# Kernel tuning notes

Hardware: AMD Instinct MI355X
Metric: run time of the kernel (lower is better)

Reference implementation:

```python
import jax, jax.numpy as jnp
import numpy as np

B, S, D, H, DQK, DH = 2, 2048, 1024, 16, 64, 64

def setup_inputs() -> dict:
    key = jax.random.key(0)
    ks = jax.random.split(key, 9)
    return {
        "x":  jax.random.normal(ks[0], (B, S, D), jnp.float32),
        "Wq": jax.random.normal(ks[1], (H, D, DQK), jnp.float32) * (D ** -0.5),
        "bq": jax.random.normal(ks[2], (H, DQK), jnp.float32) * 0.02,
        "Wk": jax.random.normal(ks[3], (H, D, DQK), jnp.float32) * (D ** -0.5),
        "bk": jax.random.normal(ks[4], (H, DQK), jnp.float32) * 0.02,
        "Wv": jax.random.normal(ks[5], (H, D, DH), jnp.float32) * (D ** -0.5),
        "bv": jax.random.normal(ks[6], (H, DH), jnp.float32) * 0.02,
        "Wo": jax.random.normal(ks[7], (D, D), jnp.float32) * (D ** -0.5),
        "bo": jax.random.normal(ks[8], (D,), jnp.float32) * 0.02,
    }

def reference(x, Wq, bq, Wk, bk, Wv, bv, Wo, bo):
    b, s, d = x.shape
    # per-head projections, all heads batched: [B,H,S,*]
    Q = jnp.einsum('bsd,hde->bhse', x, Wq) + bq[None, :, None, :]
    K = jnp.einsum('bsd,hde->bhse', x, Wk) + bk[None, :, None, :]
    V = jnp.einsum('bsd,hde->bhse', x, Wv) + bv[None, :, None, :]
    scores = jnp.einsum('bhse,bhte->bhst', Q, K) * (Q.shape[-1] ** -0.5)
    causal = jnp.tril(jnp.ones((s, s), bool))
    scores = jnp.where(causal, scores, -jnp.inf)  # mask add as in torch code
    attn = jax.nn.softmax(scores, axis=-1)        # dropout p=0 (eval)
    out = jnp.einsum('bhst,bhtd->bhsd', attn, V)
    # concat heads along feature dim (head order matches torch.cat)
    out = out.transpose(0, 2, 1, 3).reshape(b, s, -1)
    return out @ Wo + bo
```

## Files before the change

### kernel.cpp

```cpp
#include <hip/hip_runtime.h>
#include <stdint.h>

typedef __attribute__((ext_vector_type(8))) short bh8;
typedef __attribute__((ext_vector_type(4))) float f32x4;
typedef __attribute__((ext_vector_type(4))) unsigned short u16x4;
typedef __attribute__((ext_vector_type(8))) unsigned short u16x8;
typedef __attribute__((ext_vector_type(2))) unsigned int u32x2;

#define DEVI static __device__ __forceinline__

constexpr int B_ = 2, S_ = 2048, D_ = 1024, H_ = 16, E_ = 64;

constexpr size_t OFF_XB  = 0;
constexpr size_t OFF_WQT = OFF_XB  + (size_t)B_*S_*D_;
constexpr size_t OFF_WKT = OFF_WQT + (size_t)H_*E_*D_;
constexpr size_t OFF_WVT = OFF_WKT + (size_t)H_*E_*D_;
constexpr size_t OFF_WOT = OFF_WVT + (size_t)H_*E_*D_;
constexpr size_t OFF_Q   = OFF_WOT + (size_t)D_*D_;
constexpr size_t OFF_K   = OFF_Q   + (size_t)B_*H_*S_*E_;
constexpr size_t OFF_VT  = OFF_K   + (size_t)B_*H_*S_*E_;
constexpr size_t OFF_O   = OFF_VT  + (size_t)B_*H_*S_*E_;

DEVI unsigned short f2bf(float f) {
    union { float f; unsigned u; } v; v.f = f;
    unsigned u = v.u;
    return (unsigned short)((u + 0x7fffu + ((u >> 16) & 1u)) >> 16);
}

DEVI unsigned cvt_pk_bf16(float lo, float hi) {
    unsigned r;
    asm("v_cvt_pk_bf16_f32 %0, %1, %2" : "=v"(r) : "v"(lo), "v"(hi));
    return r;
}

DEVI void gload16(const void* g, void* l) {
    __builtin_amdgcn_global_load_lds(
        (const __attribute__((address_space(1))) unsigned int*)g,
        (__attribute__((address_space(3))) unsigned int*)l, 16, 0, 0);
}

DEVI f32x4 mfma16(bh8 a, bh8 b, f32x4 c) {
    return __builtin_amdgcn_mfma_f32_16x16x32_bf16(a, b, c, 0, 0, 0);
}

template<int N> DEVI void vm_barrier() {
    asm volatile("s_waitcnt vmcnt(%0)" :: "i"(N) : "memory");
    __builtin_amdgcn_s_barrier();
    __builtin_amdgcn_sched_barrier(0);
}
DEVI void post_barrier() {
    __builtin_amdgcn_sched_barrier(0);
    __builtin_amdgcn_s_barrier();
    __builtin_amdgcn_sched_barrier(0);
}

__global__ __launch_bounds__(256) void k_convert_x(const float* __restrict__ x,
                                                   unsigned short* __restrict__ ws) {
    const int i = blockIdx.x * 256 + threadIdx.x;
    const float4 v = ((const float4*)x)[i];
    u16x4 o = { f2bf(v.x), f2bf(v.y), f2bf(v.z), f2bf(v.w) };
    *(u16x4*)(ws + OFF_XB + (size_t)i * 4) = o;
}

__global__ __launch_bounds__(256) void k_transpose_w(const float* __restrict__ Wq,
                                                     const float* __restrict__ Wk,
                                                     const float* __restrict__ Wv,
                                                     const float* __restrict__ Wo,
                                                     unsigned short* __restrict__ ws) {
    const int xi = blockIdx.x;
    const int z  = blockIdx.y;
    const int t  = threadIdx.x;
    __shared__ __align__(16) unsigned short tile[64][72];

    const float* src; unsigned short* dst;
    int inCols, inBase, outBase;
    if (z < 3) {
        src = (z == 0) ? Wq : (z == 1) ? Wk : Wv;
        dst = ws + ((z == 0) ? OFF_WQT : (z == 1) ? OFF_WKT : OFF_WVT);
        inCols = 64;
        inBase = xi * 64 * 64;
        const int h = xi >> 4, dt = xi & 15;
        outBase = h * 65536 + dt * 64;
    } else {
        src = Wo; dst = ws + OFF_WOT;
        inCols = 1024;
        const int et = xi >> 4, dt = xi & 15;
        inBase  = (dt * 64) * 1024 + et * 64;
        outBase = (et * 64) * 1024 + dt * 64;
    }
#pragma unroll
    for (int v = 0; v < 4; ++v) {
        const int flat = v * 256 + t;
        const int i = flat >> 4, j4 = (flat & 15) * 4;
        const float4 val = *(const float4*)(src + inBase + i * inCols + j4);
        tile[i][j4 + 0] = f2bf(val.x);
        tile[i][j4 + 1] = f2bf(val.y);
        tile[i][j4 + 2] = f2bf(val.z);
        tile[i][j4 + 3] = f2bf(val.w);
    }
    __syncthreads();
    const int j = t >> 2, iseg = (t & 3) * 16;
    u16x8 p0, p1;
#pragma unroll
    for (int u = 0; u < 8; ++u) p0[u] = tile[iseg + u][j];
#pragma unroll
    for (int u = 0; u < 8; ++u) p1[u] = tile[iseg + 8 + u][j];
    *(u16x8*)(dst + outBase + (size_t)j * 1024 + iseg)     = p0;
    *(u16x8*)(dst + outBase + (size_t)j * 1024 + iseg + 8) = p1;
}

DEVI void qkv_stA(const unsigned short* Ap, unsigned short* lds, int kt, int mh, int ks,
                  int lane, int w, int lr, int lg) {
    const int b = kt & 1;
    const int mfrag = (w >> 2) * 8 + mh * 4 + (w & 3);
    gload16(Ap + (size_t)(mfrag * 16 + lr) * D_ + kt * 64 + ks * 32 + lg * 8,
            lds + b * 16384 + (mfrag * 2 + ks) * 512 + lane * 8);
}
DEVI void qkv_stB(const unsigned short* Bp, unsigned short* lds, int kt, int ks,
                  int lane, int w, int lr, int lg) {
    const int b = kt & 1;
#pragma unroll
    for (int u = 0; u < 2; ++u) {
        const int nfrag = w * 2 + u;
        gload16(Bp + (size_t)(nfrag * 16 + lr) * D_ + kt * 64 + ks * 32 + lg * 8,
                lds + 32768 + b * 16384 + (nfrag * 2 + ks) * 512 + lane * 8);
    }
}
DEVI bh8 qkv_ldA(const unsigned short* lds, int b, int mfrag, int ks, int lane) {
    return *(const bh8*)(lds + b * 16384 + (mfrag * 2 + ks) * 512 + lane * 8);
}
DEVI bh8 qkv_ldB(const unsigned short* lds, int b, int nfrag, int ks, int lane) {
    return *(const bh8*)(lds + 32768 + b * 16384 + (nfrag * 2 + ks) * 512 + lane * 8);
}

template<int V0, int V1, int V2, int V3, bool S0, bool S123>
DEVI void qkv_ktile(int kt, const unsigned short* Ap, const unsigned short* Bp,
                    unsigned short* lds, int lane, int w, int lr, int lg,
                    int wm, int wn, f32x4 (&acc)[8][4]) {
    const int b = kt & 1;
    bh8 af[4], bf[4];
    vm_barrier<V0>();
#pragma unroll
    for (int n = 0; n < 4; ++n) bf[n] = qkv_ldB(lds, b, wn * 4 + n, 0, lane);
#pragma unroll
    for (int q = 0; q < 4; ++q) af[q] = qkv_ldA(lds, b, wm * 8 + q, 0, lane);
    if (S0) qkv_stA(Ap, lds, kt + 1, 1, 1, lane, w, lr, lg);
    __builtin_amdgcn_s_setprio(1);
#pragma unroll
    for (int q = 0; q < 4; ++q)
#pragma unroll
        for (int n = 0; n < 4; ++n) acc[q][n] = mfma16(af[q], bf[n], acc[q][n]);
    __builtin_amdgcn_s_setprio(0);
    __builtin_amdgcn_sched_barrier(0);
    vm_barrier<V1>();
#pragma unroll
    for (int q = 0; q < 4; ++q) af[q] = qkv_ldA(lds, b, wm * 8 + 4 + q, 0, lane);
    if (S123) {
        qkv_stA(Ap, lds, kt + 2, 0, 0, lane, w, lr, lg);
        qkv_stB(Bp, lds, kt + 2, 0, lane, w, lr, lg);
    }
    __builtin_amdgcn_s_setprio(1);
#pragma unroll
    for (int q = 0; q < 4; ++q)
#pragma unroll
        for (int n = 0; n < 4; ++n) acc[4 + q][n] = mfma16(af[q], bf[n], acc[4 + q][n]);
    __builtin_amdgcn_s_setprio(0);
    __builtin_amdgcn_sched_barrier(0);
    vm_barrier<V2>();
#pragma unroll
    for (int n = 0; n < 4; ++n) bf[n] = qkv_ldB(lds, b, wn * 4 + n, 1, lane);
#pragma unroll
    for (int q = 0; q < 4; ++q) af[q] = qkv_ldA(lds, b, wm * 8 + q, 1, lane);
    if (S123) qkv_stA(Ap, lds, kt + 2, 1, 0, lane, w, lr, lg);
    __builtin_amdgcn_s_setprio(1);
#pragma unroll
    for (int q = 0; q < 4; ++q)
#pragma unroll
        for (int n = 0; n < 4; ++n) acc[q][n] = mfma16(af[q], bf[n], acc[q][n]);
    __builtin_amdgcn_s_setprio(0);
    __builtin_amdgcn_sched_barrier(0);
    vm_barrier<V3>();
#pragma unroll
    for (int q = 0; q < 4; ++q) af[q] = qkv_ldA(lds, b, wm * 8 + 4 + q, 1, lane);
    if (S123) {
        qkv_stA(Ap, lds, kt + 2, 0, 1, lane, w, lr, lg);
        qkv_stB(Bp, lds, kt + 2, 1, lane, w, lr, lg);
    }
    __builtin_amdgcn_s_setprio(1);
#pragma unroll
    for (int q = 0; q < 4; ++q)
#pragma unroll
        for (int n = 0; n < 4; ++n) acc[4 + q][n] = mfma16(af[q], bf[n], acc[4 + q][n]);
    __builtin_amdgcn_s_setprio(0);
    __builtin_amdgcn_sched_barrier(0);
}

__global__ __launch_bounds__(512, 2) void k_qkv(unsigned short* __restrict__ ws,
                                                const float* __restrict__ bq,
                                                const float* __restrict__ bk,
                                                const float* __restrict__ bv) {
    const int flat  = blockIdx.x;
    const int idx   = flat >> 3;
    const int stile = (flat & 7) * 2 + (idx & 1);
    const int ntile = idx >> 1;
    const unsigned short* Ap = ws + OFF_XB  + (size_t)stile * 256 * D_;
    const unsigned short* Bp = ws + OFF_WQT + (size_t)ntile * 256 * D_;

    __shared__ __align__(16) unsigned short lds[65536];
    const int tid = threadIdx.x, lane = tid & 63, w = tid >> 6;
    const int lr = lane & 15, lg = lane >> 4;
    const int wm = w >> 2, wn = w & 3;

    f32x4 acc[8][4];
#pragma unroll
    for (int i = 0; i < 8; ++i)
#pragma unroll
        for (int j = 0; j < 4; ++j) acc[i][j] = (f32x4){0.f, 0.f, 0.f, 0.f};

    qkv_stA(Ap, lds, 0, 0, 0, lane, w, lr, lg);
    qkv_stB(Bp, lds, 0, 0, lane, w, lr, lg);
    qkv_stA(Ap, lds, 0, 1, 0, lane, w, lr, lg);
    qkv_stA(Ap, lds, 0, 0, 1, lane, w, lr, lg);
    qkv_stB(Bp, lds, 0, 1, lane, w, lr, lg);
    qkv_stA(Ap, lds, 0, 1, 1, lane, w, lr, lg);
    qkv_stA(Ap, lds, 1, 0, 0, lane, w, lr, lg);
    qkv_stB(Bp, lds, 1, 0, lane, w, lr, lg);
    qkv_stA(Ap, lds, 1, 1, 0, lane, w, lr, lg);
    qkv_stA(Ap, lds, 1, 0, 1, lane, w, lr, lg);
    qkv_stB(Bp, lds, 1, 1, lane, w, lr, lg);

    for (int kt = 0; kt < 14; ++kt)
        qkv_ktile<12, 12, 12, 12, true, true>(kt, Ap, Bp, lds, lane, w, lr, lg, wm, wn, acc);
    qkv_ktile<12, 12, 9, 8, true, false>(14, Ap, Bp, lds, lane, w, lr, lg, wm, wn, acc);
    qkv_ktile<5, 4, 1, 0, false, false>(15, Ap, Bp, lds, lane, w, lr, lg, wm, wn, acc);

    const int c = ntile * 4 + wn;
    const int mat = c >> 4, h = c & 15;
    const float* bias = ((mat == 0) ? bq : (mat == 1) ? bk : bv) + h * 64;
    const int bb = stile >> 3;
    const int bh = bb * H_ + h;
#pragma unroll
    for (int mf = 0; mf < 8; ++mf) {
        const int sl = ((stile * 256 + wm * 128 + mf * 16) & (S_ - 1)) + lg * 4;
#pragma unroll
        for (int nf = 0; nf < 4; ++nf) {
            const int e = nf * 16 + lr;
            const float bia = bias[e];
            if (mat == 0) {
                u16x4 pk;
#pragma unroll
                for (int r = 0; r < 4; ++r)
                    pk[r] = f2bf((acc[mf][nf][r] + bia) * 0.1803368801f);
                *(u16x4*)(ws + OFF_Q + ((size_t)(bh * E_ + e)) * S_ + sl) = pk;
            } else if (mat == 2) {
                u16x4 pk;
#pragma unroll
                for (int r = 0; r < 4; ++r) pk[r] = f2bf(acc[mf][nf][r] + bia);
                *(u16x4*)(ws + OFF_VT + ((size_t)(bh * E_ + e)) * S_ + sl) = pk;
            } else {
#pragma unroll
                for (int r = 0; r < 4; ++r)
                    ws[OFF_K + ((size_t)bh * S_ + sl + r) * E_ + e] =
                        f2bf(acc[mf][nf][r] + bia);
            }
        }
    }
}

DEVI void gemm_tile_128x128(const unsigned short* __restrict__ A,
                            const unsigned short* __restrict__ Bw,
                            unsigned short* lds,
                            f32x4 acc[2][8]) {
    const int lane = threadIdx.x & 63;
    const int w    = threadIdx.x >> 6;
    const int lr = lane & 15, lg = lane >> 4;
    const unsigned short* a0 = A  + (size_t)((w * 2 + 0) * 16 + lr) * D_ + lg * 8;
    const unsigned short* a1 = A  + (size_t)((w * 2 + 1) * 16 + lr) * D_ + lg * 8;
    const unsigned short* b0 = Bw + (size_t)((w * 2 + 0) * 16 + lr) * D_ + lg * 8;
    const unsigned short* b1 = Bw + (size_t)((w * 2 + 1) * 16 + lr) * D_ + lg * 8;
    const int oA0 = (w * 2 + 0) * 512, oA1 = (w * 2 + 1) * 512;
    const int oB0 = 4096 + oA0,        oB1 = 4096 + oA1;

    auto stage = [&](int ks, int bufi) {
        unsigned short* base = lds + bufi * 8192;
        gload16(a0 + ks * 32, base + oA0);
        gload16(a1 + ks * 32, base + oA1);
        gload16(b0 + ks * 32, base + oB0);
        gload16(b1 + ks * 32, base + oB1);
    };

    stage(0, 0); stage(1, 1);
    for (int ks = 0; ks < 32; ++ks) {
        if (ks < 31) vm_barrier<4>();
        else         vm_barrier<0>();
        if (ks + 2 < 32) stage(ks + 2, (ks + 2) % 3);
        const unsigned short* base = lds + (ks % 3) * 8192;
        bh8 af0 = *(const bh8*)(base + (w * 2 + 0) * 512 + lane * 8);
        bh8 af1 = *(const bh8*)(base + (w * 2 + 1) * 512 + lane * 8);
#pragma unroll
        for (int nt = 0; nt < 8; ++nt) {
            bh8 bf = *(const bh8*)(base + 4096 + nt * 512 + lane * 8);
            acc[0][nt] = mfma16(af0, bf, acc[0][nt]);
            acc[1][nt] = mfma16(af1, bf, acc[1][nt]);
        }
        __builtin_amdgcn_sched_barrier(0);
    }
}

__global__ __launch_bounds__(256, 4) void k_attn(unsigned short* __restrict__ ws) {
    const int flat = blockIdx.x;
    const int j    = flat & 31;
    const int qt   = 31 - (flat >> 5);
    const int bh   = (j & 7) * 4 + (j >> 3);
    const int lane = threadIdx.x & 63, w = threadIdx.x >> 6;
    const int lr = lane & 15, lg = lane >> 4;
    const unsigned short* Qp = ws + OFF_Q  + (size_t)bh * E_ * S_;
    const unsigned short* Kp = ws + OFF_K  + (size_t)bh * S_ * E_;
    const unsigned short* Vp = ws + OFF_VT + (size_t)bh * E_ * S_;
    __shared__ __align__(16) unsigned short ldsK[2][8 * 512];
    __shared__ __align__(16) unsigned short ldsV[2][8 * 512];
    __shared__ __align__(16) unsigned short ldsP[4 * 1024];

    const int qbase = qt * 64 + w * 16;
    bh8 qf[2];
#pragma unroll
    for (int kg = 0; kg < 2; ++kg) {
        bh8 t;
#pragma unroll
        for (int i = 0; i < 8; ++i)
            t[i] = (short)Qp[(size_t)(kg * 32 + lg * 8 + i) * S_ + qbase + lr];
        qf[kg] = t;
    }

    f32x4 o[4];
    float m = -3.0e38f, l = 0.f;
#pragma unroll
    for (int i = 0; i < 4; ++i) o[i] = (f32x4){0.f, 0.f, 0.f, 0.f};

    auto stage = [&](int kt, int bufi) {
        const int sk0 = kt * 64;
#pragma unroll
        for (int u = 0; u < 2; ++u) {
            const int blk = w * 2 + u;
            const int ct = blk >> 1, kg = blk & 1;
            gload16(Kp + (size_t)(sk0 + ct * 16 + lr) * E_ + kg * 32 + lg * 8,
                    &ldsK[bufi][blk * 512]);
            gload16(Vp + (size_t)(ct * 16 + lr) * S_ + sk0 + kg * 32 + lg * 8,
                    &ldsV[bufi][blk * 512]);
        }
    };

    unsigned short* Pw = ldsP + w * 1024;

    stage(0, 0);
    if (qt >= 1) stage(1, 1);

    for (int kt = 0; kt <= qt; ++kt) {
        if (kt < qt) vm_barrier<4>();
        else         vm_barrier<0>();
        const int cur = kt & 1;
        const unsigned short* Kc = ldsK[cur];
        const unsigned short* Vc = ldsV[cur];

        f32x4 sc[4];
#pragma unroll
        for (int ct = 0; ct < 4; ++ct) sc[ct] = (f32x4){0.f, 0.f, 0.f, 0.f};
#pragma unroll
        for (int ct = 0; ct < 4; ++ct)
#pragma unroll
            for (int kg = 0; kg < 2; ++kg) {
                bh8 kf = *(const bh8*)(Kc + (ct * 2 + kg) * 512 + lane * 8);
                sc[ct] = mfma16(kf, qf[kg], sc[ct]);
            }
        if (kt == qt) {
#pragma unroll
            for (int ct = 0; ct < 4; ++ct) {
                const int skl = ct * 16 + lg * 4;
#pragma unroll
                for (int r = 0; r < 4; ++r)
                    if (skl + r > w * 16 + lr) sc[ct][r] = -3.0e38f;
            }
        }
        float mx = fmaxf(fmaxf(sc[0][0], sc[0][1]), fmaxf(sc[0][2], sc[0][3]));
#pragma unroll
        for (int ct = 1; ct < 4; ++ct)
            mx = fmaxf(mx, fmaxf(fmaxf(sc[ct][0], sc[ct][1]),
                                 fmaxf(sc[ct][2], sc[ct][3])));
        mx = fmaxf(mx, __shfl_xor(mx, 16, 64));
        mx = fmaxf(mx, __shfl_xor(mx, 32, 64));
        const bool need = mx > m + 8.0f;
        if (__any(need)) {
            const float mn = need ? mx : m;
            const float sf = __builtin_amdgcn_exp2f(m - mn);
            m = mn;
            l *= sf;
#pragma unroll
            for (int r = 0; r < 4; ++r) {
                const float sfq = __shfl(sf, (lane & 48) + lg * 4 + r, 64);
#pragma unroll
                for (int et = 0; et < 4; ++et) o[et][r] *= sfq;
            }
        }
        float rs = 0.f;
#pragma unroll
        for (int ct = 0; ct < 4; ++ct)
#pragma unroll
            for (int r = 0; r < 4; ++r) {
                float p = __builtin_amdgcn_exp2f(sc[ct][r] - m);
                sc[ct][r] = p;
                rs += p;
            }
        rs += __shfl_xor(rs, 16, 64);
        rs += __shfl_xor(rs, 32, 64);
        l += rs;
#pragma unroll
        for (int ct = 0; ct < 4; ++ct) {
            u32x2 pk = { cvt_pk_bf16(sc[ct][0], sc[ct][1]),
                         cvt_pk_bf16(sc[ct][2], sc[ct][3]) };
            const int addr = (ct >> 1) * 512 +
                             ((((ct & 1) * 2) + (lg >> 1)) * 16 + lr) * 8 + (lg & 1) * 4;
            *(u32x2*)(Pw + addr) = pk;
        }
#pragma unroll
        for (int skg = 0; skg < 2; ++skg) {
            bh8 pf = *(const bh8*)(Pw + skg * 512 + lane * 8);
#pragma unroll
            for (int et = 0; et < 4; ++et) {
                bh8 vf = *(const bh8*)(Vc + (et * 2 + skg) * 512 + lane * 8);
                o[et] = mfma16(pf, vf, o[et]);
            }
        }
        post_barrier();
        if (kt + 2 <= qt) stage(kt + 2, cur);
    }
    const int b = bh >> 4, hh = bh & 15;
#pragma unroll
    for (int r = 0; r < 4; ++r) {
        const float lq = __shfl(l, (lane & 48) + lg * 4 + r, 64);
        const float inv = 1.0f / lq;
        const int s = qbase + lg * 4 + r;
#pragma unroll
        for (int et = 0; et < 4; ++et)
            ws[OFF_O + ((size_t)(b * S_ + s)) * D_ + hh * E_ + et * 16 + lr] =
                f2bf(o[et][r] * inv);
    }
}

__global__ __launch_bounds__(256, 3) void k_oproj(const unsigned short* __restrict__ ws,
                                                  const float* __restrict__ bo,
                                                  float* __restrict__ out) {
    const int flat  = blockIdx.x;
    const int idx   = flat >> 3;
    const int stile = (flat & 7) * 4 + (idx & 3);
    const int ntile = idx >> 2;
    const unsigned short* A  = ws + OFF_O   + (size_t)stile * 128 * D_;
    const unsigned short* Bw = ws + OFF_WOT + (size_t)ntile * 128 * D_;
    __shared__ __align__(16) unsigned short lds[3 * 8192];
    f32x4 acc[2][8];
#pragma unroll
    for (int i = 0; i < 2; ++i)
#pragma unroll
        for (int j = 0; j < 8; ++j) acc[i][j] = (f32x4){0.f, 0.f, 0.f, 0.f};

    gemm_tile_128x128(A, Bw, lds, acc);

    const int lane = threadIdx.x & 63, w = threadIdx.x >> 6;
    const int lr = lane & 15, lg = lane >> 4;
    const int r0 = stile * 128 + w * 32;
#pragma unroll
    for (int mt = 0; mt < 2; ++mt)
#pragma unroll
        for (int nt = 0; nt < 8; ++nt) {
            const int e = ntile * 128 + nt * 16 + lr;
            const float bia = bo[e];
#pragma unroll
            for (int r = 0; r < 4; ++r)
                out[(size_t)(r0 + mt * 16 + lg * 4 + r) * D_ + e] = acc[mt][nt][r] + bia;
        }
}

extern "C" void kernel_launch(void* const* d_in, const int* in_sizes, int n_in,
                              void* d_out, int out_size, void* d_ws, size_t ws_size,
                              hipStream_t stream) {
    const float* x  = (const float*)d_in[0];
    const float* Wq = (const float*)d_in[1];
    const float* bq = (const float*)d_in[2];
    const float* Wk = (const float*)d_in[3];
    const float* bk = (const float*)d_in[4];
    const float* Wv = (const float*)d_in[5];
    const float* bv = (const float*)d_in[6];
    const float* Wo = (const float*)d_in[7];
    const float* bo = (const float*)d_in[8];
    float* out = (float*)d_out;
    unsigned short* ws = (unsigned short*)d_ws;

    k_convert_x<<<dim3((B_ * S_ * D_) / 4 / 256), 256, 0, stream>>>(x, ws);
    k_transpose_w<<<dim3(256, 4), 256, 0, stream>>>(Wq, Wk, Wv, Wo, ws);
    k_qkv<<<dim3(192), 512, 0, stream>>>(ws, bq, bk, bv);
    k_attn<<<dim3(1024), 256, 0, stream>>>(ws);
    k_oproj<<<dim3(256), 256, 0, stream>>>(ws, bo, out);
}
```

Baseline: 118.9 us.

## Process 128 query rows per attention block to reuse K/V tiles

The attention kernel now gives each wave two 16-row query sub-tiles (128 queries per block) instead of one, so every K/V tile staged into LDS feeds twice as many MFMAs. The grid is halved to 512 blocks and the causal mask is applied over the last two key tiles. This cuts global K/V traffic and LDS reads per query, at the cost of more registers (occupancy bound lowered to 3), a larger P buffer and coarser causal load balancing.

```diff
diff --git a/kernel.cpp b/kernel.cpp
--- a/kernel.cpp
+++ b/kernel.cpp
@@ -307,10 +307,10 @@
     }
 }
 
-__global__ __launch_bounds__(256, 4) void k_attn(unsigned short* __restrict__ ws) {
+__global__ __launch_bounds__(256, 3) void k_attn(unsigned short* __restrict__ ws) {
     const int flat = blockIdx.x;
     const int j    = flat & 31;
-    const int qt   = 31 - (flat >> 5);
+    const int qt2  = 15 - (flat >> 5);
     const int bh   = (j & 7) * 4 + (j >> 3);
     const int lane = threadIdx.x & 63, w = threadIdx.x >> 6;
     const int lr = lane & 15, lg = lane >> 4;
@@ -319,23 +319,27 @@
     const unsigned short* Vp = ws + OFF_VT + (size_t)bh * E_ * S_;
     __shared__ __align__(16) unsigned short ldsK[2][8 * 512];
     __shared__ __align__(16) unsigned short ldsV[2][8 * 512];
-    __shared__ __align__(16) unsigned short ldsP[4 * 1024];
-
-    const int qbase = qt * 64 + w * 16;
-    bh8 qf[2];
-#pragma unroll
-    for (int kg = 0; kg < 2; ++kg) {
-        bh8 t;
-#pragma unroll
-        for (int i = 0; i < 8; ++i)
-            t[i] = (short)Qp[(size_t)(kg * 32 + lg * 8 + i) * S_ + qbase + lr];
-        qf[kg] = t;
-    }
-
-    f32x4 o[4];
-    float m = -3.0e38f, l = 0.f;
-#pragma unroll
-    for (int i = 0; i < 4; ++i) o[i] = (f32x4){0.f, 0.f, 0.f, 0.f};
+    __shared__ __align__(16) unsigned short ldsP[4 * 2048];
+
+    const int qbase = qt2 * 128 + w * 32;
+    bh8 qf[2][2];
+#pragma unroll
+    for (int mq = 0; mq < 2; ++mq)
+#pragma unroll
+        for (int kg = 0; kg < 2; ++kg) {
+            bh8 t;
+#pragma unroll
+            for (int i = 0; i < 8; ++i)
+                t[i] = (short)Qp[(size_t)(kg * 32 + lg * 8 + i) * S_ + qbase + mq * 16 + lr];
+            qf[mq][kg] = t;
+        }
+
+    f32x4 o[2][4];
+    float m[2] = {-3.0e38f, -3.0e38f}, l[2] = {0.f, 0.f};
+#pragma unroll
+    for (int mq = 0; mq < 2; ++mq)
+#pragma unroll
+        for (int i = 0; i < 4; ++i) o[mq][i] = (f32x4){0.f, 0.f, 0.f, 0.f};
 
     auto stage = [&](int kt, int bufi) {
         const int sk0 = kt * 64;
@@ -350,100 +354,125 @@
         }
     };
 
-    unsigned short* Pw = ldsP + w * 1024;
+    unsigned short* Pw = ldsP + w * 2048;
+    const int nkt = 2 * qt2 + 2;
 
     stage(0, 0);
-    if (qt >= 1) stage(1, 1);
-
-    for (int kt = 0; kt <= qt; ++kt) {
-        if (kt < qt) vm_barrier<4>();
-        else         vm_barrier<0>();
+    if (nkt > 1) stage(1, 1);
+
+    for (int kt = 0; kt < nkt; ++kt) {
+        if (kt + 1 < nkt) vm_barrier<4>();
+        else              vm_barrier<0>();
         const int cur = kt & 1;
         const unsigned short* Kc = ldsK[cur];
         const unsigned short* Vc = ldsV[cur];
 
-        f32x4 sc[4];
-#pragma unroll
-        for (int ct = 0; ct < 4; ++ct) sc[ct] = (f32x4){0.f, 0.f, 0.f, 0.f};
+        f32x4 sc[2][4];
+#pragma unroll
+        for (int mq = 0; mq < 2; ++mq)
+#pragma unroll
+            for (int ct = 0; ct < 4; ++ct) sc[mq][ct] = (f32x4){0.f, 0.f, 0.f, 0.f};
 #pragma unroll
         for (int ct = 0; ct < 4; ++ct)
 #pragma unroll
             for (int kg = 0; kg < 2; ++kg) {
                 bh8 kf = *(const bh8*)(Kc + (ct * 2 + kg) * 512 + lane * 8);
-                sc[ct] = mfma16(kf, qf[kg], sc[ct]);
+                sc[0][ct] = mfma16(kf, qf[0][kg], sc[0][ct]);
+                sc[1][ct] = mfma16(kf, qf[1][kg], sc[1][ct]);
             }
-        if (kt == qt) {
+        if (kt >= 2 * qt2) {
+            const int dq = qt2 * 128 - kt * 64;
+#pragma unroll
+            for (int mq = 0; mq < 2; ++mq) {
+                const int qo = w * 32 + mq * 16 + lr + dq;
+#pragma unroll
+                for (int ct = 0; ct < 4; ++ct) {
+                    const int skl = ct * 16 + lg * 4;
+#pragma unroll
+                    for (int r = 0; r < 4; ++r)
+                        if (skl + r > qo) sc[mq][ct][r] = -3.0e38f;
+                }
+            }
+        }
+        float mx[2];
+#pragma unroll
+        for (int mq = 0; mq < 2; ++mq) {
+            float v = fmaxf(fmaxf(sc[mq][0][0], sc[mq][0][1]),
+                            fmaxf(sc[mq][0][2], sc[mq][0][3]));
+#pragma unroll
+            for (int ct = 1; ct < 4; ++ct)
+                v = fmaxf(v, fmaxf(fmaxf(sc[mq][ct][0], sc[mq][ct][1]),
+                                   fmaxf(sc[mq][ct][2], sc[mq][ct][3])));
+            v = fmaxf(v, __shfl_xor(v, 16, 64));
+            mx[mq] = fmaxf(v, __shfl_xor(v, 32, 64));
+        }
+        const bool need0 = mx[0] > m[0] + 8.0f, need1 = mx[1] > m[1] + 8.0f;
+        if (__any(need0 | need1)) {
+#pragma unroll
+            for (int mq = 0; mq < 2; ++mq) {
+                const bool nd = mq == 0 ? need0 : need1;
+                const float mn = nd ? mx[mq] : m[mq];
+                const float sf = __builtin_amdgcn_exp2f(m[mq] - mn);
+                m[mq] = mn;
+                l[mq] *= sf;
+#pragma unroll
+                for (int r = 0; r < 4; ++r) {
+                    const float sfq = __shfl(sf, (lane & 48) + lg * 4 + r, 64);
+#pragma unroll
+                    for (int et = 0; et < 4; ++et) o[mq][et][r] *= sfq;
+                }
+            }
+        }
+#pragma unroll
+        for (int mq = 0; mq < 2; ++mq) {
+            float rs = 0.f;
+#pragma unroll
+            for (int ct = 0; ct < 4; ++ct)
+#pragma unroll
+                for (int r = 0; r < 4; ++r) {
+                    float p = __builtin_amdgcn_exp2f(sc[mq][ct][r] - m[mq]);
+                    sc[mq][ct][r] = p;
+                    rs += p;
+                }
+            rs += __shfl_xor(rs, 16, 64);
+            rs += __shfl_xor(rs, 32, 64);
+            l[mq] += rs;
 #pragma unroll
             for (int ct = 0; ct < 4; ++ct) {
-                const int skl = ct * 16 + lg * 4;
-#pragma unroll
-                for (int r = 0; r < 4; ++r)
-                    if (skl + r > w * 16 + lr) sc[ct][r] = -3.0e38f;
+                u32x2 pk = { cvt_pk_bf16(sc[mq][ct][0], sc[mq][ct][1]),
+                             cvt_pk_bf16(sc[mq][ct][2], sc[mq][ct][3]) };
+                const int addr = mq * 1024 + (ct >> 1) * 512 +
+                                 ((((ct & 1) * 2) + (lg >> 1)) * 16 + lr) * 8 + (lg & 1) * 4;
+                *(u32x2*)(Pw + addr) = pk;
             }
         }
-        float mx = fmaxf(fmaxf(sc[0][0], sc[0][1]), fmaxf(sc[0][2], sc[0][3]));
-#pragma unroll
-        for (int ct = 1; ct < 4; ++ct)
-            mx = fmaxf(mx, fmaxf(fmaxf(sc[ct][0], sc[ct][1]),
-                                 fmaxf(sc[ct][2], sc[ct][3])));
-        mx = fmaxf(mx, __shfl_xor(mx, 16, 64));
-        mx = fmaxf(mx, __shfl_xor(mx, 32, 64));
-        const bool need = mx > m + 8.0f;
-        if (__any(need)) {
-            const float mn = need ? mx : m;
-            const float sf = __builtin_amdgcn_exp2f(m - mn);
-            m = mn;
-            l *= sf;
-#pragma unroll
-            for (int r = 0; r < 4; ++r) {
-                const float sfq = __shfl(sf, (lane & 48) + lg * 4 + r, 64);
-#pragma unroll
-                for (int et = 0; et < 4; ++et) o[et][r] *= sfq;
-            }
-        }
-        float rs = 0.f;
-#pragma unroll
-        for (int ct = 0; ct < 4; ++ct)
-#pragma unroll
-            for (int r = 0; r < 4; ++r) {
-                float p = __builtin_amdgcn_exp2f(sc[ct][r] - m);
-                sc[ct][r] = p;
-                rs += p;
-            }
-        rs += __shfl_xor(rs, 16, 64);
-        rs += __shfl_xor(rs, 32, 64);
-        l += rs;
-#pragma unroll
-        for (int ct = 0; ct < 4; ++ct) {
-            u32x2 pk = { cvt_pk_bf16(sc[ct][0], sc[ct][1]),
-                         cvt_pk_bf16(sc[ct][2], sc[ct][3]) };
-            const int addr = (ct >> 1) * 512 +
-                             ((((ct & 1) * 2) + (lg >> 1)) * 16 + lr) * 8 + (lg & 1) * 4;
-            *(u32x2*)(Pw + addr) = pk;
-        }
 #pragma unroll
         for (int skg = 0; skg < 2; ++skg) {
-            bh8 pf = *(const bh8*)(Pw + skg * 512 + lane * 8);
+            bh8 pf0 = *(const bh8*)(Pw + 0 * 1024 + skg * 512 + lane * 8);
+            bh8 pf1 = *(const bh8*)(Pw + 1 * 1024 + skg * 512 + lane * 8);
 #pragma unroll
             for (int et = 0; et < 4; ++et) {
                 bh8 vf = *(const bh8*)(Vc + (et * 2 + skg) * 512 + lane * 8);
-                o[et] = mfma16(pf, vf, o[et]);
+                o[0][et] = mfma16(pf0, vf, o[0][et]);
+                o[1][et] = mfma16(pf1, vf, o[1][et]);
             }
         }
         post_barrier();
-        if (kt + 2 <= qt) stage(kt + 2, cur);
+        if (kt + 2 < nkt) stage(kt + 2, cur);
     }
     const int b = bh >> 4, hh = bh & 15;
 #pragma unroll
-    for (int r = 0; r < 4; ++r) {
-        const float lq = __shfl(l, (lane & 48) + lg * 4 + r, 64);
-        const float inv = 1.0f / lq;
-        const int s = qbase + lg * 4 + r;
-#pragma unroll
-        for (int et = 0; et < 4; ++et)
-            ws[OFF_O + ((size_t)(b * S_ + s)) * D_ + hh * E_ + et * 16 + lr] =
-                f2bf(o[et][r] * inv);
-    }
+    for (int mq = 0; mq < 2; ++mq)
+#pragma unroll
+        for (int r = 0; r < 4; ++r) {
+            const float lq = __shfl(l[mq], (lane & 48) + lg * 4 + r, 64);
+            const float inv = 1.0f / lq;
+            const int s = qbase + mq * 16 + lg * 4 + r;
+#pragma unroll
+            for (int et = 0; et < 4; ++et)
+                ws[OFF_O + ((size_t)(b * S_ + s)) * D_ + hh * E_ + et * 16 + lr] =
+                    f2bf(o[mq][et][r] * inv);
+        }
 }
 
 __global__ __launch_bounds__(256, 3) void k_oproj(const unsigned short* __restrict__ ws,
@@ -497,6 +526,6 @@
     k_convert_x<<<dim3((B_ * S_ * D_) / 4 / 256), 256, 0, stream>>>(x, ws);
     k_transpose_w<<<dim3(256, 4), 256, 0, stream>>>(Wq, Wk, Wv, Wo, ws);
     k_qkv<<<dim3(192), 512, 0, stream>>>(ws, bq, bk, bv);
-    k_attn<<<dim3(1024), 256, 0, stream>>>(ws);
+    k_attn<<<dim3(512), 256, 0, stream>>>(ws);
     k_oproj<<<dim3(256), 256, 0, stream>>>(ws, bo, out);
 }
```

Result: slower. 124.3 us (+4.5%).
